# Kernel tuning notes

Hardware: AMD Instinct MI355X
Metric: run time of the kernel (lower is better)

Reference implementation:

```python
import jax, jax.numpy as jnp
from jax import lax
import numpy as np

V = 50000          # num_word; embedding table has V+1 rows
D = 512            # embedding_dim / d_model
H = 8              # nhead
FF = 2048          # dim_feedforward (hidden_dim)
L = 32             # num_label (incl START/STOP)
START, STOP = L - 2, L - 1
S = 2048           # sentence length
NEG = -10000.0


def setup_inputs() -> dict:
    k = jax.random.split(jax.random.key(0), 10)
    def rn(key, shape, s=0.02):
        return jax.random.normal(key, shape, jnp.float32) * s
    transitions = jax.random.normal(k[8], (L, L), jnp.float32)
    transitions = transitions.at[START, :].set(NEG).at[:, STOP].set(NEG)
    return {
        "sentence": jax.random.randint(k[0], (S,), 0, V + 1),
        "embed": rn(k[1], (V + 1, D), 1.0),
        "Wqkv": rn(k[2], (3 * D, D)), "bqkv": jnp.zeros((3 * D,), jnp.float32),
        "Wo": rn(k[3], (D, D)), "bo": jnp.zeros((D,), jnp.float32),
        "ln1_g": jnp.ones((D,), jnp.float32), "ln1_b": jnp.zeros((D,), jnp.float32),
        "W1": rn(k[4], (FF, D)), "b1": jnp.zeros((FF,), jnp.float32),
        "W2": rn(k[5], (D, FF)), "b2": jnp.zeros((D,), jnp.float32),
        "ln2_g": jnp.ones((D,), jnp.float32), "ln2_b": jnp.zeros((D,), jnp.float32),
        "Wt": rn(k[6], (L, D)), "bt": jnp.zeros((L,), jnp.float32),
        "transitions": transitions,
    }


def _ln(x, g, b):
    m = jnp.mean(x, -1, keepdims=True)
    v = jnp.var(x, -1, keepdims=True)
    return (x - m) * lax.rsqrt(v + 1e-5) * g + b


def _transformer_feats(sentence, embed, Wqkv, bqkv, Wo, bo, ln1_g, ln1_b,
                       W1, b1, W2, b2, ln2_g, ln2_b, Wt, bt):
    x = embed[sentence]                                   # [S, D]
    qkv = x @ Wqkv.T + bqkv                               # [S, 3D]
    q, k, v = jnp.split(qkv, 3, axis=-1)
    to_heads = lambda t: t.reshape(S, H, D // H).transpose(1, 0, 2)  # [H, S, dh]
    q, k, v = to_heads(q), to_heads(k), to_heads(v)
    att = jax.nn.softmax(jnp.einsum('hsd,htd->hst', q, k) / np.float32(np.sqrt(D // H)), axis=-1)
    o = jnp.einsum('hst,htd->hsd', att, v).transpose(1, 0, 2).reshape(S, D)
    # post-norm TransformerEncoderLayer (eval mode: dropout off), relu FFN
    x = _ln(x + o @ Wo.T + bo, ln1_g, ln1_b)
    ff = jax.nn.relu(x @ W1.T + b1) @ W2.T + b2
    x = _ln(x + ff, ln2_g, ln2_b)
    return x @ Wt.T + bt                                  # [S, L] emission scores


def _viterbi(feats, transitions):
    init = jnp.full((L,), NEG, jnp.float32).at[START].set(0.0)
    def step(prev, emit):
        scores = prev[None, :] + transitions              # [next_tag, prev_tag]
        bp = jnp.argmax(scores, axis=1)                   # best prev tag per next tag
        return jnp.max(scores, axis=1) + emit, bp
    last, bps = lax.scan(step, init, feats)               # bps: [S, L]
    terminal = last + transitions[STOP]
    best = jnp.argmax(terminal)
    def back(tag, bp):
        return bp[tag], tag
    _, path = lax.scan(back, best, bps, reverse=True)     # path[t] = best tag at step t
    return terminal[best], path


def reference(sentence, embed, Wqkv, bqkv, Wo, bo, ln1_g, ln1_b,
              W1, b1, W2, b2, ln2_g, ln2_b, Wt, bt, transitions):
    feats = _transformer_feats(sentence, embed, Wqkv, bqkv, Wo, bo, ln1_g, ln1_b,
                               W1, b1, W2, b2, ln2_g, ln2_b, Wt, bt)
    score, path = _viterbi(feats, transitions)
    return score, path
```

## Files before the change

### kernel.cpp

```cpp
#include <hip/hip_runtime.h>
#include <cstddef>

#define S_LEN 2048
#define D_MODEL 512
#define NHEAD 8
#define DH 64
#define FF_DIM 2048
#define L_TAGS 32
#define START_TAG 30
#define STOP_TAG 31
#define NEGV (-10000.0f)

typedef unsigned int uint2v __attribute__((ext_vector_type(2)));
typedef __attribute__((ext_vector_type(8))) short short8v;
typedef __attribute__((ext_vector_type(4))) float f32x4;

union U8 { uint4 u; short8v s; };

__device__ __forceinline__ unsigned short f2bf(float f) {
  unsigned u = __float_as_uint(f);
  u += 0x7fff + ((u >> 16) & 1);
  return (unsigned short)(u >> 16);
}
__device__ __forceinline__ unsigned cvtpk(float lo, float hi) {
  unsigned r;
  asm("v_cvt_pk_bf16_f32 %0, %1, %2" : "=v"(r) : "v"(lo), "v"(hi));
  return r;
}

__global__ __launch_bounds__(256) void k_f2h(const float* __restrict__ src,
                                             short* __restrict__ dst, int n8) {
  int i = blockIdx.x * 256 + threadIdx.x;
  if (i >= n8) return;
  f32x4 a = *(const f32x4*)(src + (size_t)i * 8);
  f32x4 b = *(const f32x4*)(src + (size_t)i * 8 + 4);
  U8 t;
  t.u.x = cvtpk(a[0], a[1]); t.u.y = cvtpk(a[2], a[3]);
  t.u.z = cvtpk(b[0], b[1]); t.u.w = cvtpk(b[2], b[3]);
  *(short8v*)(dst + (size_t)i * 8) = t.s;
}

__global__ __launch_bounds__(128) void k_embed(const int* __restrict__ sent,
                                               const float* __restrict__ embed,
                                               float* __restrict__ x,
                                               short* __restrict__ xh) {
  int s = blockIdx.x;
  int d = threadIdx.x * 4;
  size_t off = (size_t)s * D_MODEL + d;
  float4 v = *(const float4*)(embed + (size_t)sent[s] * D_MODEL + d);
  *(float4*)(x + off) = v;
  uint2v t;
  t[0] = cvtpk(v.x, v.y);
  t[1] = cvtpk(v.z, v.w);
  *(uint2v*)(xh + off) = t;
}

template <int RT, bool RELU, bool OBF>
__global__ __launch_bounds__(256, 2) void k_gemm_bf(const short* __restrict__ A,
                                                    const short* __restrict__ B,
                                                    const float* __restrict__ bias,
                                                    void* __restrict__ Cp,
                                                    int M, int N, int K) {
  constexpr int BM = RT * 32;
  constexpr int CH = (BM * 8) / 256;
  __shared__ __align__(16) short As[2][BM * 64];
  __shared__ __align__(16) short Bs[2][BM * 64];
  const int tid = threadIdx.x;
  const int bm = blockIdx.y * BM, bn = blockIdx.x * BM;
  const int w = tid >> 6, lane = tid & 63;
  const int wr = w >> 1, wc = w & 1;
  const int fr = lane & 15, kg = lane >> 4;
  const int srow = (RT == 4) ? (tid >> 1) : (tid >> 2);
  const int sc0 = (RT == 4) ? ((tid & 1) * 4) : ((tid & 3) * 2);
  const int swz = srow & 7;
  const short* gA = A + (size_t)(bm + srow) * K + sc0 * 8;
  const short* gB = B + (size_t)(bn + srow) * K + sc0 * 8;
  short8v ra[CH], rb[CH];
  f32x4 acc[RT][RT] = {};

  auto loadg = [&](int k0) {
#pragma unroll
    for (int c = 0; c < CH; ++c) {
      ra[c] = *(const short8v*)(gA + k0 + c * 8);
      rb[c] = *(const short8v*)(gB + k0 + c * 8);
    }
  };
  auto storeb = [&](int b) {
    short* dA = &As[b][srow * 64];
    short* dB = &Bs[b][srow * 64];
#pragma unroll
    for (int c = 0; c < CH; ++c) {
      *(short8v*)(dA + (((sc0 + c) ^ swz) << 3)) = ra[c];
      *(short8v*)(dB + (((sc0 + c) ^ swz) << 3)) = rb[c];
    }
  };

  loadg(0);
  storeb(0);
  __syncthreads();
  int cur = 0;
  const int fswz = fr & 7;
  for (int k0 = 0; k0 < K; k0 += 64) {
    const bool more = (k0 + 64) < K;
    if (more) loadg(k0 + 64);
    const short* rA = &As[cur][(wr * (RT * 16) + fr) * 64];
    const short* rB = &Bs[cur][(wc * (RT * 16) + fr) * 64];
#pragma unroll
    for (int ks = 0; ks < 2; ++ks) {
      const int co = ((ks * 4 + kg) ^ fswz) << 3;
      short8v af[RT], bf[RT];
#pragma unroll
      for (int rt = 0; rt < RT; ++rt) af[rt] = *(const short8v*)(rA + rt * 16 * 64 + co);
#pragma unroll
      for (int ct = 0; ct < RT; ++ct) bf[ct] = *(const short8v*)(rB + ct * 16 * 64 + co);
#pragma unroll
      for (int rt = 0; rt < RT; ++rt)
#pragma unroll
        for (int ct = 0; ct < RT; ++ct)
          acc[rt][ct] = __builtin_amdgcn_mfma_f32_16x16x32_bf16(af[rt], bf[ct], acc[rt][ct], 0, 0, 0);
    }
    if (more) storeb(cur ^ 1);
    __syncthreads();
    cur ^= 1;
  }
#pragma unroll
  for (int rt = 0; rt < RT; ++rt) {
#pragma unroll
    for (int ct = 0; ct < RT; ++ct) {
      f32x4 v = acc[rt][ct];
      const int row0 = bm + wr * (RT * 16) + rt * 16 + kg * 4;
      const int col = bn + wc * (RT * 16) + ct * 16 + fr;
      const float bs = bias[col];
#pragma unroll
      for (int j = 0; j < 4; ++j) {
        float o = v[j] + bs;
        if (RELU) o = fmaxf(o, 0.f);
        if (OBF)
          ((short*)Cp)[(size_t)(row0 + j) * N + col] = (short)f2bf(o);
        else
          ((float*)Cp)[(size_t)(row0 + j) * N + col] = o;
      }
    }
  }
}

__global__ __launch_bounds__(256) void k_attn(const short* __restrict__ qkv,
                                              short* __restrict__ ob) {
  __shared__ __align__(16) short Ks[2][64 * 64];
  __shared__ __align__(16) short Vt[2][64 * 72];
  __shared__ __align__(16) short Pl[4][16 * 72];
  const int tid = threadIdx.x;
  const int b = blockIdx.x;
  const int h = b & 7;
  const int bq = (b >> 3) * 64;
  const int wq = tid >> 6, lane = tid & 63;
  const int fr = lane & 15, kg = lane >> 4;
  short8v qf[2];
  {
    const short* qsrc = qkv + (size_t)(bq + wq * 16 + fr) * 1536 + h * DH;
    qf[0] = *(const short8v*)(qsrc + kg * 8);
    qf[1] = *(const short8v*)(qsrc + 32 + kg * 8);
  }
  float m[4], l[4];
  f32x4 oac[4] = {};
#pragma unroll
  for (int j = 0; j < 4; ++j) { m[j] = -1e30f; l[j] = 0.f; }

  const int srow = tid >> 2, sc0 = (tid & 3) * 2;
  const int kpair = tid & 31, dgrp = tid >> 5;
  short8v kr0, kr1, va, vb;
  auto loadt = [&](int kt) {
    const short* kbase = qkv + (size_t)(kt * 64 + srow) * 1536 + 512 + h * DH;
    kr0 = *(const short8v*)(kbase + sc0 * 8);
    kr1 = *(const short8v*)(kbase + sc0 * 8 + 8);
    const short* vbase = qkv + (size_t)(kt * 64 + 2 * kpair) * 1536 + 1024 + h * DH + dgrp * 8;
    va = *(const short8v*)(vbase);
    vb = *(const short8v*)(vbase + 1536);
  };
  auto storet = [&](int cu) {
    short* dk = &Ks[cu][srow * 64];
    *(short8v*)(dk + ((sc0 ^ (srow & 7)) << 3)) = kr0;
    *(short8v*)(dk + (((sc0 + 1) ^ (srow & 7)) << 3)) = kr1;
#pragma unroll
    for (int i = 0; i < 8; ++i) {
      unsigned u = ((unsigned)(unsigned short)va[i]) |
                   (((unsigned)(unsigned short)vb[i]) << 16);
      *(unsigned*)&Vt[cu][(dgrp * 8 + i) * 72 + 2 * kpair] = u;
    }
  };

  loadt(0);
  int cur = 0;
  for (int kt = 0; kt < 32; ++kt) {
    storet(cur);
    __syncthreads();
    if (kt < 31) loadt(kt + 1);
    f32x4 sac[4] = {};
#pragma unroll
    for (int ks = 0; ks < 2; ++ks) {
#pragma unroll
      for (int ct = 0; ct < 4; ++ct) {
        const int row = ct * 16 + fr;
        short8v bfr = *(const short8v*)&Ks[cur][row * 64 + (((ks * 4 + kg) ^ (row & 7)) << 3)];
        sac[ct] = __builtin_amdgcn_mfma_f32_16x16x32_bf16(qf[ks], bfr, sac[ct], 0, 0, 0);
      }
    }
#pragma unroll
    for (int ct = 0; ct < 4; ++ct) sac[ct] *= 0.125f;
    float pv[4][4];
#pragma unroll
    for (int j = 0; j < 4; ++j) {
      float v = fmaxf(fmaxf(sac[0][j], sac[1][j]), fmaxf(sac[2][j], sac[3][j]));
#pragma unroll
      for (int off = 1; off < 16; off <<= 1) v = fmaxf(v, __shfl_xor(v, off, 64));
      float mn = fmaxf(m[j], v);
      float f = __expf(m[j] - mn);
      m[j] = mn;
      float rs = 0.f;
#pragma unroll
      for (int ct = 0; ct < 4; ++ct) {
        pv[ct][j] = __expf(sac[ct][j] - mn);
        rs += pv[ct][j];
      }
#pragma unroll
      for (int off = 1; off < 16; off <<= 1) rs += __shfl_xor(rs, off, 64);
      l[j] = l[j] * f + rs;
#pragma unroll
      for (int ct = 0; ct < 4; ++ct) oac[ct][j] *= f;
    }
#pragma unroll
    for (int ct = 0; ct < 4; ++ct)
#pragma unroll
      for (int j = 0; j < 4; ++j)
        Pl[wq][(kg * 4 + j) * 72 + ct * 16 + fr] = (short)f2bf(pv[ct][j]);
#pragma unroll
    for (int ks = 0; ks < 2; ++ks) {
      short8v paf = *(const short8v*)&Pl[wq][fr * 72 + ks * 32 + kg * 8];
#pragma unroll
      for (int ct = 0; ct < 4; ++ct) {
        short8v vf = *(const short8v*)&Vt[cur][(ct * 16 + fr) * 72 + ks * 32 + kg * 8];
        oac[ct] = __builtin_amdgcn_mfma_f32_16x16x32_bf16(paf, vf, oac[ct], 0, 0, 0);
      }
    }
    cur ^= 1;
  }
#pragma unroll
  for (int j = 0; j < 4; ++j) {
    float inv = 1.f / l[j];
    const int q = bq + wq * 16 + kg * 4 + j;
#pragma unroll
    for (int ct = 0; ct < 4; ++ct)
      ob[(size_t)q * D_MODEL + h * DH + ct * 16 + fr] = (short)f2bf(oac[ct][j] * inv);
  }
}

__global__ __launch_bounds__(128) void k_ln(const float* __restrict__ a,
                                            const float* __restrict__ r,
                                            const float* __restrict__ g,
                                            const float* __restrict__ b,
                                            float* __restrict__ out,
                                            short* __restrict__ outh) {
  __shared__ float red[2];
  const int row = blockIdx.x, tid = threadIdx.x;
  const size_t off = (size_t)row * D_MODEL + tid * 4;
  float4 av = *(const float4*)(a + off);
  float4 rv = *(const float4*)(r + off);
  float v0 = av.x + rv.x, v1 = av.y + rv.y, v2 = av.z + rv.z, v3 = av.w + rv.w;
  float s = v0 + v1 + v2 + v3;
#pragma unroll
  for (int d = 1; d < 64; d <<= 1) s += __shfl_xor(s, d, 64);
  if ((tid & 63) == 0) red[tid >> 6] = s;
  __syncthreads();
  float mean = (red[0] + red[1]) * (1.f / 512.f);
  __syncthreads();
  float d0 = v0 - mean, d1 = v1 - mean, d2 = v2 - mean, d3 = v3 - mean;
  float sq = d0 * d0 + d1 * d1 + d2 * d2 + d3 * d3;
#pragma unroll
  for (int d = 1; d < 64; d <<= 1) sq += __shfl_xor(sq, d, 64);
  if ((tid & 63) == 0) red[tid >> 6] = sq;
  __syncthreads();
  float inv = rsqrtf((red[0] + red[1]) * (1.f / 512.f) + 1e-5f);
  float4 gv = *(const float4*)(g + tid * 4);
  float4 bv = *(const float4*)(b + tid * 4);
  float4 o;
  o.x = d0 * inv * gv.x + bv.x;
  o.y = d1 * inv * gv.y + bv.y;
  o.z = d2 * inv * gv.z + bv.z;
  o.w = d3 * inv * gv.w + bv.w;
  *(float4*)(out + off) = o;
  if (outh) {
    uint2v t;
    t[0] = cvtpk(o.x, o.y);
    t[1] = cvtpk(o.z, o.w);
    *(uint2v*)(outh + off) = t;
  }
}

__global__ __launch_bounds__(256) void k_feats(const float* __restrict__ x2,
                                               const float* __restrict__ Wt,
                                               const float* __restrict__ bt,
                                               float* __restrict__ feats) {
  const int tid = threadIdx.x;
  const int s = blockIdx.x * 8 + (tid >> 5);
  const int l = tid & 31;
  const float* xr = x2 + (size_t)s * D_MODEL;
  const float* wr = Wt + (size_t)l * D_MODEL;
  float acc = 0.f;
#pragma unroll 8
  for (int k = 0; k < D_MODEL; k += 4) {
    float4 xv = *(const float4*)(xr + k);
    float4 wv = *(const float4*)(wr + k);
    acc += xv.x * wv.x + xv.y * wv.y + xv.z * wv.z + xv.w * wv.w;
  }
  feats[s * L_TAGS + l] = acc + bt[l];
}

__global__ __launch_bounds__(64) void k_scan1(const float* __restrict__ feats,
                                              const float* __restrict__ T,
                                              float* __restrict__ P) {
  __shared__ float S[2][32];
  const int c = blockIdx.x >> 4;
  const int l = threadIdx.x;
  const int n = l & 31, pl = l >> 5;
  const int p = (blockIdx.x & 15) * 2 + pl;
  float Trow[32];
#pragma unroll
  for (int q = 0; q < 32; ++q) Trow[q] = T[n * 32 + q];
  const int tbase = c * 32;
  float er[4];
#pragma unroll
  for (int i = 0; i < 4; ++i) er[i] = feats[(tbase + i) * 32 + n];
  float a = T[n * 32 + p] + er[0];
  S[pl][n] = a;
  const float* fp = feats + (size_t)(tbase + 4) * 32 + n;
  er[0] = fp[0]; fp += 32;
  for (int u = 1; u < 32; ++u) {
    float e = er[u & 3];
    float enew = fp[0]; fp += 32;
    const float4* Sv = (const float4*)&S[pl][0];
    float g[32];
#pragma unroll
    for (int j4 = 0; j4 < 8; ++j4) {
      float4 sv = Sv[j4];
      g[j4 * 4 + 0] = sv.x + Trow[j4 * 4 + 0];
      g[j4 * 4 + 1] = sv.y + Trow[j4 * 4 + 1];
      g[j4 * 4 + 2] = sv.z + Trow[j4 * 4 + 2];
      g[j4 * 4 + 3] = sv.w + Trow[j4 * 4 + 3];
    }
#pragma unroll
    for (int st = 1; st < 32; st <<= 1)
#pragma unroll
      for (int j = 0; j < 32; j += 2 * st) g[j] = fmaxf(g[j], g[j + st]);
    a = g[0] + e;
    S[pl][n] = a;
    er[u & 3] = enew;
  }
  P[(size_t)c * 1024 + n * 32 + p] = a;
}

__global__ __launch_bounds__(64) void k_scan2(const float* __restrict__ P,
                                              const float* __restrict__ T,
                                              float* __restrict__ alphas,
                                              float* __restrict__ out,
                                              int* __restrict__ bestp) {
  __shared__ float Sa[32];
  const int l = threadIdx.x, n = l & 31, half = l >> 5;
  float a = (n == START_TAG) ? 0.f : NEGV;
  const float* pbase = P + n * 32 + half * 16;
  float4 pr[4];
#pragma unroll
  for (int j = 0; j < 4; ++j) pr[j] = *(const float4*)(pbase + j * 4);
  for (int c = 0; c < 64; ++c) {
    float4 nx[4];
#pragma unroll
    for (int j = 0; j < 4; ++j)
      nx[j] = *(const float4*)(pbase + (size_t)(c + 1) * 1024 + j * 4);
    alphas[(size_t)(c * 32) * 32 + n] = a;
    Sa[n] = a;
    const float4* Sv = (const float4*)&Sa[half * 16];
    float g[16];
#pragma unroll
    for (int j = 0; j < 4; ++j) {
      float4 sv = Sv[j];
      g[j * 4 + 0] = pr[j].x + sv.x;
      g[j * 4 + 1] = pr[j].y + sv.y;
      g[j * 4 + 2] = pr[j].z + sv.z;
      g[j * 4 + 3] = pr[j].w + sv.w;
    }
#pragma unroll
    for (int st = 1; st < 16; st <<= 1)
#pragma unroll
      for (int j = 0; j < 16; j += 2 * st) g[j] = fmaxf(g[j], g[j + st]);
    uint2v r = __builtin_amdgcn_permlane32_swap(__float_as_uint(g[0]),
                                                __float_as_uint(g[0]), false, false);
    a = fmaxf(__uint_as_float(r[0]), __uint_as_float(r[1]));
#pragma unroll
    for (int j = 0; j < 4; ++j) pr[j] = nx[j];
  }
  float term = a + T[STOP_TAG * 32 + n];
  float bv = term;
  int bi = n;
#pragma unroll
  for (int d = 1; d < 32; d <<= 1) {
    float ov = __shfl_xor(bv, d, 64);
    int oi = __shfl_xor(bi, d, 64);
    if (ov > bv || (ov == bv && oi < bi)) { bv = ov; bi = oi; }
  }
  if (l == 0) { out[0] = bv; *bestp = bi; }
}

__global__ __launch_bounds__(64) void k_scan3(const float* __restrict__ feats,
                                              const float* __restrict__ T,
                                              float* __restrict__ alphas) {
  __shared__ float Sa[32];
  const int c = blockIdx.x, l = threadIdx.x, n = l & 31, half = l >> 5;
  float Tr[16];
#pragma unroll
  for (int j = 0; j < 16; ++j) Tr[j] = T[n * 32 + half * 16 + j];
  const int tbase = c * 32;
  float a = alphas[(size_t)tbase * 32 + n];
  float er[4];
#pragma unroll
  for (int i = 0; i < 4; ++i) er[i] = feats[(tbase + i) * 32 + n];
  const float* fp = feats + (size_t)(tbase + 4) * 32 + n;
  Sa[n] = a;
  for (int u = 0; u < 31; ++u) {
    float e = er[u & 3];
    float enew = fp[0]; fp += 32;
    const float4* Sv = (const float4*)&Sa[half * 16];
    float4 s0 = Sv[0], s1 = Sv[1], s2 = Sv[2], s3 = Sv[3];
    float g[16] = {s0.x + Tr[0],  s0.y + Tr[1],  s0.z + Tr[2],  s0.w + Tr[3],
                   s1.x + Tr[4],  s1.y + Tr[5],  s1.z + Tr[6],  s1.w + Tr[7],
                   s2.x + Tr[8],  s2.y + Tr[9],  s2.z + Tr[10], s2.w + Tr[11],
                   s3.x + Tr[12], s3.y + Tr[13], s3.z + Tr[14], s3.w + Tr[15]};
#pragma unroll
    for (int st = 1; st < 16; st <<= 1)
#pragma unroll
      for (int j = 0; j < 16; j += 2 * st) g[j] = fmaxf(g[j], g[j + st]);
    uint2v r = __builtin_amdgcn_permlane32_swap(__float_as_uint(g[0]),
                                                __float_as_uint(g[0]), false, false);
    a = fmaxf(__uint_as_float(r[0]), __uint_as_float(r[1])) + e;
    alphas[(size_t)(tbase + u + 1) * 32 + n] = a;
    Sa[n] = a;
    er[u & 3] = enew;
  }
}

__global__ __launch_bounds__(256) void k_vit_bp(const float* __restrict__ alphas,
                                                const float* __restrict__ T,
                                                unsigned char* __restrict__ bp) {
  __shared__ float Ts[32][33];
  __shared__ float Al[8][32];
  const int tid = threadIdx.x;
  for (int i = tid; i < 1024; i += 256) Ts[i >> 5][i & 31] = T[i];
  const int t0 = blockIdx.x * 8;
  Al[tid >> 5][tid & 31] = alphas[t0 * 32 + tid];
  __syncthreads();
  const int tl = tid >> 5, n = tid & 31;
  float best = -3e38f;
  int bi = 0;
#pragma unroll
  for (int p = 0; p < 32; ++p) {
    float v = Al[tl][p] + Ts[n][p];
    if (v > best) { best = v; bi = p; }
  }
  bp[(size_t)(t0 + tl) * 32 + n] = (unsigned char)bi;
}

__global__ __launch_bounds__(256) void k_trace1(const unsigned char* __restrict__ bp,
                                                unsigned char* __restrict__ cand,
                                                unsigned char* __restrict__ amap) {
  __shared__ unsigned bplw[256];
  __shared__ unsigned cndw[256];
  const int c = blockIdx.x, tid = threadIdx.x;
  bplw[tid] = ((const unsigned*)(bp + (size_t)c * 1024))[tid];
  __syncthreads();
  if (tid < 32) {
    const unsigned char* bl = (const unsigned char*)bplw;
    unsigned char* cn = (unsigned char*)cndw;
    int tg = tid;
    cn[tid * 32 + 31] = (unsigned char)tg;
    for (int j = 31; j >= 1; --j) {
      tg = bl[j * 32 + tg];
      cn[tid * 32 + (j - 1)] = (unsigned char)tg;
    }
    amap[c * 32 + tid] = bl[tg];
  }
  __syncthreads();
  ((unsigned*)(cand + (size_t)c * 1024))[tid] = cndw[tid];
}

__global__ __launch_bounds__(256) void k_trace2(const unsigned char* __restrict__ amap,
                                                const unsigned char* __restrict__ cand,
                                                const int* __restrict__ bestp,
                                                float* __restrict__ outp) {
  __shared__ unsigned char Am[64][32];
  __shared__ unsigned char et[64];
  const int tid = threadIdx.x;
  ((unsigned*)&Am[0][0])[tid] = ((const unsigned*)amap)[tid];
  ((unsigned*)&Am[32][0])[tid] = ((const unsigned*)amap)[tid + 256];
  __syncthreads();
  for (int d = 1; d < 64; d <<= 1) {
    unsigned char tmpv[8];
#pragma unroll
    for (int i = 0; i < 8; ++i) {
      int id = tid + 256 * i;
      int cc = id >> 5, e = id & 31;
      tmpv[i] = (cc + d < 64) ? Am[cc][Am[cc + d][e]] : Am[cc][e];
    }
    __syncthreads();
#pragma unroll
    for (int i = 0; i < 8; ++i) {
      int id = tid + 256 * i;
      Am[id >> 5][id & 31] = tmpv[i];
    }
    __syncthreads();
  }
  const int best = *bestp;
  if (tid < 64) et[tid] = (tid == 63) ? (unsigned char)best : Am[tid + 1][best];
  __syncthreads();
#pragma unroll
  for (int i = 0; i < 8; ++i) {
    int t = tid + 256 * i;
    int cc = t >> 5, j = t & 31;
    outp[1 + t] = (float)cand[(size_t)cc * 1024 + (size_t)et[cc] * 32 + j];
  }
}

extern "C" void kernel_launch(void* const* d_in, const int* in_sizes, int n_in,
                              void* d_out, int out_size, void* d_ws, size_t ws_size,
                              hipStream_t stream) {
  (void)in_sizes; (void)n_in; (void)out_size; (void)ws_size;
  const int* sent = (const int*)d_in[0];
  const float* embed = (const float*)d_in[1];
  const float* Wqkv = (const float*)d_in[2];
  const float* bqkv = (const float*)d_in[3];
  const float* Wo = (const float*)d_in[4];
  const float* bo = (const float*)d_in[5];
  const float* g1 = (const float*)d_in[6];
  const float* b1n = (const float*)d_in[7];
  const float* W1 = (const float*)d_in[8];
  const float* b1f = (const float*)d_in[9];
  const float* W2 = (const float*)d_in[10];
  const float* b2f = (const float*)d_in[11];
  const float* g2 = (const float*)d_in[12];
  const float* b2n = (const float*)d_in[13];
  const float* Wt = (const float*)d_in[14];
  const float* bt = (const float*)d_in[15];
  const float* T = (const float*)d_in[16];
  float* out = (float*)d_out;

  float* ws = (float*)d_ws;
  const size_t M1 = 1u << 20;
  float* x = ws;
  short* xh = (short*)(ws + M1);
  short* qkvh = (short*)(ws + 3 * M1 / 2);
  short* obh = (short*)(ws + M1);
  float* yb = ws + 3 * M1 / 2;
  float* x1 = ws + 3 * M1;
  short* x1h = (short*)(ws + 5 * M1 / 2);
  short* ffbh = (short*)ws;
  float* zb = ws + 2 * M1;
  float* x2 = ws;
  short* wqkvh = (short*)(ws + 4 * M1);
  short* woh = wqkvh + 786432;
  short* w1h = woh + 262144;
  short* w2h = w1h + 1048576;
  float* feats = ws + 4 * M1 + 3 * M1 / 2;
  float* alphas = feats + 2048 * 32 + 64;
  float* P = alphas + 2049 * 32 + 64;
  int* bestp = (int*)(P + 65 * 1024 + 64);
  unsigned char* bp = (unsigned char*)(bestp + 64);
  unsigned char* cand = bp + 2048 * 32;
  unsigned char* amap = cand + 2048 * 32;

  k_f2h<<<dim3(384), dim3(256), 0, stream>>>(Wqkv, wqkvh, 98304);
  k_f2h<<<dim3(128), dim3(256), 0, stream>>>(Wo, woh, 32768);
  k_f2h<<<dim3(512), dim3(256), 0, stream>>>(W1, w1h, 131072);
  k_f2h<<<dim3(512), dim3(256), 0, stream>>>(W2, w2h, 131072);
  k_embed<<<dim3(2048), dim3(128), 0, stream>>>(sent, embed, x, xh);
  k_gemm_bf<4, false, true><<<dim3(12, 16), dim3(256), 0, stream>>>(xh, wqkvh, bqkv, qkvh, 2048, 1536, 512);
  k_attn<<<dim3(256), dim3(256), 0, stream>>>(qkvh, obh);
  k_gemm_bf<2, false, false><<<dim3(8, 32), dim3(256), 0, stream>>>(obh, woh, bo, yb, 2048, 512, 512);
  k_ln<<<dim3(2048), dim3(128), 0, stream>>>(x, yb, g1, b1n, x1, x1h);
  k_gemm_bf<4, true, true><<<dim3(16, 16), dim3(256), 0, stream>>>(x1h, w1h, b1f, ffbh, 2048, 2048, 512);
  k_gemm_bf<2, false, false><<<dim3(8, 32), dim3(256), 0, stream>>>(ffbh, w2h, b2f, zb, 2048, 512, 2048);
  k_ln<<<dim3(2048), dim3(128), 0, stream>>>(x1, zb, g2, b2n, x2, (short*)nullptr);
  k_feats<<<dim3(256), dim3(256), 0, stream>>>(x2, Wt, bt, feats);
  k_scan1<<<dim3(1024), dim3(64), 0, stream>>>(feats, T, P);
  k_scan2<<<dim3(1), dim3(64), 0, stream>>>(P, T, alphas, out, bestp);
  k_scan3<<<dim3(64), dim3(64), 0, stream>>>(feats, T, alphas);
  k_vit_bp<<<dim3(256), dim3(256), 0, stream>>>(alphas, T, bp);
  k_trace1<<<dim3(64), dim3(256), 0, stream>>>(bp, cand, amap);
  k_trace2<<<dim3(1), dim3(256), 0, stream>>>(amap, cand, bestp, out);
}
```

Baseline: 199.2 us.

## Fuse weight casts, embedding gather into QKV GEMM, and Viterbi backpointer tracing

Result: faster. 187.3 us (-6.0%).

```diff
diff --git a/kernel.cpp b/kernel.cpp
--- a/kernel.cpp
+++ b/kernel.cpp
@@ -28,31 +28,109 @@
   return r;
 }
 
-__global__ __launch_bounds__(256) void k_f2h(const float* __restrict__ src,
-                                             short* __restrict__ dst, int n8) {
-  int i = blockIdx.x * 256 + threadIdx.x;
-  if (i >= n8) return;
+__global__ __launch_bounds__(256) void k_f2h4(const float* __restrict__ s0, short* __restrict__ d0,
+                                              const float* __restrict__ s1, short* __restrict__ d1,
+                                              const float* __restrict__ s2, short* __restrict__ d2,
+                                              const float* __restrict__ s3, short* __restrict__ d3) {
+  const int b = blockIdx.x;
+  const float* src; short* dst; int i;
+  if (b < 384)       { src = s0; dst = d0; i = b * 256 + threadIdx.x; }
+  else if (b < 512)  { src = s1; dst = d1; i = (b - 384) * 256 + threadIdx.x; }
+  else if (b < 1024) { src = s2; dst = d2; i = (b - 512) * 256 + threadIdx.x; }
+  else               { src = s3; dst = d3; i = (b - 1024) * 256 + threadIdx.x; }
   f32x4 a = *(const f32x4*)(src + (size_t)i * 8);
-  f32x4 b = *(const f32x4*)(src + (size_t)i * 8 + 4);
+  f32x4 c = *(const f32x4*)(src + (size_t)i * 8 + 4);
   U8 t;
   t.u.x = cvtpk(a[0], a[1]); t.u.y = cvtpk(a[2], a[3]);
-  t.u.z = cvtpk(b[0], b[1]); t.u.w = cvtpk(b[2], b[3]);
+  t.u.z = cvtpk(c[0], c[1]); t.u.w = cvtpk(c[2], c[3]);
   *(short8v*)(dst + (size_t)i * 8) = t.s;
 }
 
-__global__ __launch_bounds__(128) void k_embed(const int* __restrict__ sent,
-                                               const float* __restrict__ embed,
-                                               float* __restrict__ x,
-                                               short* __restrict__ xh) {
-  int s = blockIdx.x;
-  int d = threadIdx.x * 4;
-  size_t off = (size_t)s * D_MODEL + d;
-  float4 v = *(const float4*)(embed + (size_t)sent[s] * D_MODEL + d);
-  *(float4*)(x + off) = v;
-  uint2v t;
-  t[0] = cvtpk(v.x, v.y);
-  t[1] = cvtpk(v.z, v.w);
-  *(uint2v*)(xh + off) = t;
+__global__ __launch_bounds__(256, 2) void k_gemm_qkv(const int* __restrict__ sent,
+                                                     const float* __restrict__ embed,
+                                                     const short* __restrict__ B,
+                                                     const float* __restrict__ bias,
+                                                     short* __restrict__ C,
+                                                     int N, int K) {
+  __shared__ __align__(16) short As[2][128 * 64];
+  __shared__ __align__(16) short Bs[2][128 * 64];
+  const int tid = threadIdx.x;
+  const int bm = blockIdx.y * 128, bn = blockIdx.x * 128;
+  const int w = tid >> 6, lane = tid & 63;
+  const int wr = w >> 1, wc = w & 1;
+  const int fr = lane & 15, kg = lane >> 4;
+  const int srow = tid >> 1, sc0 = (tid & 1) * 4;
+  const int swz = srow & 7;
+  const float* gA = embed + (size_t)sent[bm + srow] * K + sc0 * 8;
+  const short* gB = B + (size_t)(bn + srow) * K + sc0 * 8;
+  f32x4 ra[8];
+  short8v rb[4];
+  f32x4 acc[4][4] = {};
+
+  auto loadg = [&](int k0) {
+#pragma unroll
+    for (int c = 0; c < 4; ++c) {
+      ra[2 * c] = *(const f32x4*)(gA + k0 + c * 8);
+      ra[2 * c + 1] = *(const f32x4*)(gA + k0 + c * 8 + 4);
+      rb[c] = *(const short8v*)(gB + k0 + c * 8);
+    }
+  };
+  auto storeb = [&](int b) {
+    short* dA = &As[b][srow * 64];
+    short* dB = &Bs[b][srow * 64];
+#pragma unroll
+    for (int c = 0; c < 4; ++c) {
+      U8 ta;
+      ta.u.x = cvtpk(ra[2 * c][0], ra[2 * c][1]);
+      ta.u.y = cvtpk(ra[2 * c][2], ra[2 * c][3]);
+      ta.u.z = cvtpk(ra[2 * c + 1][0], ra[2 * c + 1][1]);
+      ta.u.w = cvtpk(ra[2 * c + 1][2], ra[2 * c + 1][3]);
+      *(short8v*)(dA + (((sc0 + c) ^ swz) << 3)) = ta.s;
+      *(short8v*)(dB + (((sc0 + c) ^ swz) << 3)) = rb[c];
+    }
+  };
+
+  loadg(0);
+  storeb(0);
+  __syncthreads();
+  int cur = 0;
+  const int fswz = fr & 7;
+  for (int k0 = 0; k0 < K; k0 += 64) {
+    const bool more = (k0 + 64) < K;
+    if (more) loadg(k0 + 64);
+    const short* rA = &As[cur][(wr * 64 + fr) * 64];
+    const short* rB = &Bs[cur][(wc * 64 + fr) * 64];
+#pragma unroll
+    for (int ks = 0; ks < 2; ++ks) {
+      const int co = ((ks * 4 + kg) ^ fswz) << 3;
+      short8v af[4], bf[4];
+#pragma unroll
+      for (int rt = 0; rt < 4; ++rt) af[rt] = *(const short8v*)(rA + rt * 16 * 64 + co);
+#pragma unroll
+      for (int ct = 0; ct < 4; ++ct) bf[ct] = *(const short8v*)(rB + ct * 16 * 64 + co);
+#pragma unroll
+      for (int rt = 0; rt < 4; ++rt)
+#pragma unroll
+        for (int ct = 0; ct < 4; ++ct)
+          acc[rt][ct] = __builtin_amdgcn_mfma_f32_16x16x32_bf16(af[rt], bf[ct], acc[rt][ct], 0, 0, 0);
+    }
+    if (more) storeb(cur ^ 1);
+    __syncthreads();
+    cur ^= 1;
+  }
+#pragma unroll
+  for (int rt = 0; rt < 4; ++rt) {
+#pragma unroll
+    for (int ct = 0; ct < 4; ++ct) {
+      f32x4 v = acc[rt][ct];
+      const int row0 = bm + wr * 64 + rt * 16 + kg * 4;
+      const int col = bn + wc * 64 + ct * 16 + fr;
+      const float bs = bias[col];
+#pragma unroll
+      for (int j = 0; j < 4; ++j)
+        C[(size_t)(row0 + j) * N + col] = (short)f2bf(v[j] + bs);
+    }
+  }
 }
 
 template <int RT, bool RELU, bool OBF>
@@ -255,6 +333,8 @@
 }
 
 __global__ __launch_bounds__(128) void k_ln(const float* __restrict__ a,
+                                            const int* __restrict__ sent,
+                                            const float* __restrict__ embed,
                                             const float* __restrict__ r,
                                             const float* __restrict__ g,
                                             const float* __restrict__ b,
@@ -263,7 +343,11 @@
   __shared__ float red[2];
   const int row = blockIdx.x, tid = threadIdx.x;
   const size_t off = (size_t)row * D_MODEL + tid * 4;
-  float4 av = *(const float4*)(a + off);
+  float4 av;
+  if (sent)
+    av = *(const float4*)(embed + (size_t)sent[row] * D_MODEL + tid * 4);
+  else
+    av = *(const float4*)(a + off);
   float4 rv = *(const float4*)(r + off);
   float v0 = av.x + rv.x, v1 = av.y + rv.y, v2 = av.z + rv.z, v3 = av.w + rv.w;
   float s = v0 + v1 + v2 + v3;
@@ -411,8 +495,12 @@
 
 __global__ __launch_bounds__(64) void k_scan3(const float* __restrict__ feats,
                                               const float* __restrict__ T,
-                                              float* __restrict__ alphas) {
+                                              const float* __restrict__ alphas,
+                                              unsigned char* __restrict__ cand,
+                                              unsigned char* __restrict__ amap) {
   __shared__ float Sa[32];
+  __shared__ unsigned char bpl[32][32];
+  __shared__ unsigned cnd[256];
   const int c = blockIdx.x, l = threadIdx.x, n = l & 31, half = l >> 5;
   float Tr[16];
 #pragma unroll
@@ -424,70 +512,47 @@
   for (int i = 0; i < 4; ++i) er[i] = feats[(tbase + i) * 32 + n];
   const float* fp = feats + (size_t)(tbase + 4) * 32 + n;
   Sa[n] = a;
-  for (int u = 0; u < 31; ++u) {
+  for (int u = 0; u < 32; ++u) {
     float e = er[u & 3];
     float enew = fp[0]; fp += 32;
     const float4* Sv = (const float4*)&Sa[half * 16];
     float4 s0 = Sv[0], s1 = Sv[1], s2 = Sv[2], s3 = Sv[3];
-    float g[16] = {s0.x + Tr[0],  s0.y + Tr[1],  s0.z + Tr[2],  s0.w + Tr[3],
+    float v[16] = {s0.x + Tr[0],  s0.y + Tr[1],  s0.z + Tr[2],  s0.w + Tr[3],
                    s1.x + Tr[4],  s1.y + Tr[5],  s1.z + Tr[6],  s1.w + Tr[7],
                    s2.x + Tr[8],  s2.y + Tr[9],  s2.z + Tr[10], s2.w + Tr[11],
                    s3.x + Tr[12], s3.y + Tr[13], s3.z + Tr[14], s3.w + Tr[15]};
+    int id[16];
+#pragma unroll
+    for (int j = 0; j < 16; ++j) id[j] = half * 16 + j;
 #pragma unroll
     for (int st = 1; st < 16; st <<= 1)
 #pragma unroll
-      for (int j = 0; j < 16; j += 2 * st) g[j] = fmaxf(g[j], g[j + st]);
-    uint2v r = __builtin_amdgcn_permlane32_swap(__float_as_uint(g[0]),
-                                                __float_as_uint(g[0]), false, false);
-    a = fmaxf(__uint_as_float(r[0]), __uint_as_float(r[1])) + e;
-    alphas[(size_t)(tbase + u + 1) * 32 + n] = a;
+      for (int j = 0; j < 16; j += 2 * st)
+        if (v[j + st] > v[j]) { v[j] = v[j + st]; id[j] = id[j + st]; }
+    uint2v rv = __builtin_amdgcn_permlane32_swap(__float_as_uint(v[0]),
+                                                 __float_as_uint(v[0]), false, false);
+    uint2v ri = __builtin_amdgcn_permlane32_swap((unsigned)id[0], (unsigned)id[0],
+                                                 false, false);
+    float v0 = __uint_as_float(rv[0]), v1 = __uint_as_float(rv[1]);
+    int i0 = (int)ri[0], i1 = (int)ri[1];
+    float wv = (v1 > v0) ? v1 : v0;
+    int wi = (v1 > v0) ? i1 : i0;
+    bpl[u][n] = (unsigned char)wi;
+    a = wv + e;
     Sa[n] = a;
     er[u & 3] = enew;
   }
-}
-
-__global__ __launch_bounds__(256) void k_vit_bp(const float* __restrict__ alphas,
-                                                const float* __restrict__ T,
-                                                unsigned char* __restrict__ bp) {
-  __shared__ float Ts[32][33];
-  __shared__ float Al[8][32];
-  const int tid = threadIdx.x;
-  for (int i = tid; i < 1024; i += 256) Ts[i >> 5][i & 31] = T[i];
-  const int t0 = blockIdx.x * 8;
-  Al[tid >> 5][tid & 31] = alphas[t0 * 32 + tid];
-  __syncthreads();
-  const int tl = tid >> 5, n = tid & 31;
-  float best = -3e38f;
-  int bi = 0;
-#pragma unroll
-  for (int p = 0; p < 32; ++p) {
-    float v = Al[tl][p] + Ts[n][p];
-    if (v > best) { best = v; bi = p; }
-  }
-  bp[(size_t)(t0 + tl) * 32 + n] = (unsigned char)bi;
-}
-
-__global__ __launch_bounds__(256) void k_trace1(const unsigned char* __restrict__ bp,
-                                                unsigned char* __restrict__ cand,
-                                                unsigned char* __restrict__ amap) {
-  __shared__ unsigned bplw[256];
-  __shared__ unsigned cndw[256];
-  const int c = blockIdx.x, tid = threadIdx.x;
-  bplw[tid] = ((const unsigned*)(bp + (size_t)c * 1024))[tid];
-  __syncthreads();
-  if (tid < 32) {
-    const unsigned char* bl = (const unsigned char*)bplw;
-    unsigned char* cn = (unsigned char*)cndw;
-    int tg = tid;
-    cn[tid * 32 + 31] = (unsigned char)tg;
-    for (int j = 31; j >= 1; --j) {
-      tg = bl[j * 32 + tg];
-      cn[tid * 32 + (j - 1)] = (unsigned char)tg;
-    }
-    amap[c * 32 + tid] = bl[tg];
-  }
-  __syncthreads();
-  ((unsigned*)(cand + (size_t)c * 1024))[tid] = cndw[tid];
+  unsigned char* cnb = (unsigned char*)cnd;
+  int tg = n;
+  cnb[n * 32 + 31] = (unsigned char)n;
+  for (int j = 31; j >= 1; --j) {
+    tg = bpl[j][tg];
+    cnb[n * 32 + (j - 1)] = (unsigned char)tg;
+  }
+  if (half == 0) amap[c * 32 + n] = bpl[0][tg];
+#pragma unroll
+  for (int i = 0; i < 4; ++i)
+    ((unsigned*)(cand + (size_t)c * 1024))[l * 4 + i] = cnd[l * 4 + i];
 }
 
 __global__ __launch_bounds__(256) void k_trace2(const unsigned char* __restrict__ amap,
@@ -552,45 +617,36 @@
 
   float* ws = (float*)d_ws;
   const size_t M1 = 1u << 20;
-  float* x = ws;
-  short* xh = (short*)(ws + M1);
-  short* qkvh = (short*)(ws + 3 * M1 / 2);
-  short* obh = (short*)(ws + M1);
-  float* yb = ws + 3 * M1 / 2;
-  float* x1 = ws + 3 * M1;
-  short* x1h = (short*)(ws + 5 * M1 / 2);
-  short* ffbh = (short*)ws;
-  float* zb = ws + 2 * M1;
-  float* x2 = ws;
-  short* wqkvh = (short*)(ws + 4 * M1);
+  short* qkvh = (short*)ws;
+  short* obh = (short*)(ws + 2 * M1);
+  float* yb = ws + 3 * M1;
+  float* x1 = ws + 4 * M1;
+  short* x1h = (short*)(ws + 5 * M1);
+  short* ffbh = (short*)(ws + 6 * M1);
+  float* zb = ws + 8 * M1;
+  float* x2 = ws + 9 * M1;
+  short* wqkvh = (short*)(ws + 10 * M1);
   short* woh = wqkvh + 786432;
   short* w1h = woh + 262144;
   short* w2h = w1h + 1048576;
-  float* feats = ws + 4 * M1 + 3 * M1 / 2;
+  float* feats = ws + 11 * M1;
   float* alphas = feats + 2048 * 32 + 64;
   float* P = alphas + 2049 * 32 + 64;
   int* bestp = (int*)(P + 65 * 1024 + 64);
-  unsigned char* bp = (unsigned char*)(bestp + 64);
-  unsigned char* cand = bp + 2048 * 32;
+  unsigned char* cand = (unsigned char*)(bestp + 64);
   unsigned char* amap = cand + 2048 * 32;
 
-  k_f2h<<<dim3(384), dim3(256), 0, stream>>>(Wqkv, wqkvh, 98304);
-  k_f2h<<<dim3(128), dim3(256), 0, stream>>>(Wo, woh, 32768);
-  k_f2h<<<dim3(512), dim3(256), 0, stream>>>(W1, w1h, 131072);
-  k_f2h<<<dim3(512), dim3(256), 0, stream>>>(W2, w2h, 131072);
-  k_embed<<<dim3(2048), dim3(128), 0, stream>>>(sent, embed, x, xh);
-  k_gemm_bf<4, false, true><<<dim3(12, 16), dim3(256), 0, stream>>>(xh, wqkvh, bqkv, qkvh, 2048, 1536, 512);
+  k_f2h4<<<dim3(1536), dim3(256), 0, stream>>>(Wqkv, wqkvh, Wo, woh, W1, w1h, W2, w2h);
+  k_gemm_qkv<<<dim3(12, 16), dim3(256), 0, stream>>>(sent, embed, wqkvh, bqkv, qkvh, 1536, 512);
   k_attn<<<dim3(256), dim3(256), 0, stream>>>(qkvh, obh);
   k_gemm_bf<2, false, false><<<dim3(8, 32), dim3(256), 0, stream>>>(obh, woh, bo, yb, 2048, 512, 512);
-  k_ln<<<dim3(2048), dim3(128), 0, stream>>>(x, yb, g1, b1n, x1, x1h);
+  k_ln<<<dim3(2048), dim3(128), 0, stream>>>(nullptr, sent, embed, yb, g1, b1n, x1, x1h);
   k_gemm_bf<4, true, true><<<dim3(16, 16), dim3(256), 0, stream>>>(x1h, w1h, b1f, ffbh, 2048, 2048, 512);
   k_gemm_bf<2, false, false><<<dim3(8, 32), dim3(256), 0, stream>>>(ffbh, w2h, b2f, zb, 2048, 512, 2048);
-  k_ln<<<dim3(2048), dim3(128), 0, stream>>>(x1, zb, g2, b2n, x2, (short*)nullptr);
+  k_ln<<<dim3(2048), dim3(128), 0, stream>>>(x1, nullptr, nullptr, zb, g2, b2n, x2, (short*)nullptr);
   k_feats<<<dim3(256), dim3(256), 0, stream>>>(x2, Wt, bt, feats);
   k_scan1<<<dim3(1024), dim3(64), 0, stream>>>(feats, T, P);
   k_scan2<<<dim3(1), dim3(64), 0, stream>>>(P, T, alphas, out, bestp);
-  k_scan3<<<dim3(64), dim3(64), 0, stream>>>(feats, T, alphas);
-  k_vit_bp<<<dim3(256), dim3(256), 0, stream>>>(alphas, T, bp);
-  k_trace1<<<dim3(64), dim3(256), 0, stream>>>(bp, cand, amap);
+  k_scan3<<<dim3(64), dim3(64), 0, stream>>>(feats, T, alphas, cand, amap);
   k_trace2<<<dim3(1), dim3(256), 0, stream>>>(amap, cand, bestp, out);
 }
```
